# Kernel tuning notes

Hardware: AMD Instinct MI355X
Metric: run time of the kernel (lower is better)

## Reference

```python
import jax, jax.numpy as jnp
import numpy as np

L = 8        # n_layers (coupling layers)
H = 128      # hidden width
B = 262144   # batch
BN_EPS = 1e-5
FLOW_EPS = 1e-4


def setup_inputs() -> dict:
    key = jax.random.key(0)
    ks = jax.random.split(key, 16)
    d = {}
    d['x'] = jax.random.normal(ks[0], (B, 2), dtype=jnp.float32)
    # weight-normalized Linear(1 -> H): direction v, magnitude g, bias b
    d['v1'] = jax.random.normal(ks[1], (L, H, 1), dtype=jnp.float32)
    d['g1'] = 1.0 + 0.1 * jax.random.normal(ks[2], (L, H), dtype=jnp.float32)
    d['b1'] = 0.1 * jax.random.normal(ks[3], (L, H), dtype=jnp.float32)
    d['bn1_g'] = 1.0 + 0.1 * jax.random.normal(ks[4], (L, H), dtype=jnp.float32)
    d['bn1_b'] = 0.1 * jax.random.normal(ks[5], (L, H), dtype=jnp.float32)
    # weight-normalized Linear(H -> H)
    d['v2'] = jax.random.normal(ks[6], (L, H, H), dtype=jnp.float32) / np.sqrt(H)
    d['g2'] = 1.0 + 0.1 * jax.random.normal(ks[7], (L, H), dtype=jnp.float32)
    d['b2'] = 0.1 * jax.random.normal(ks[8], (L, H), dtype=jnp.float32)
    d['bn2_g'] = 1.0 + 0.1 * jax.random.normal(ks[9], (L, H), dtype=jnp.float32)
    d['bn2_b'] = 0.1 * jax.random.normal(ks[10], (L, H), dtype=jnp.float32)
    # final plain Linear(H -> 2)
    d['wf'] = jax.random.normal(ks[11], (L, 2, H), dtype=jnp.float32) / np.sqrt(H)
    d['bf'] = 0.1 * jax.random.normal(ks[12], (L, 2), dtype=jnp.float32)
    return d


def _wn_linear(x, v, g, b):
    # torch weight_norm: W = g * v / ||v||_row  (norm over input dim)
    w = g[:, None] * v / jnp.linalg.norm(v, axis=1, keepdims=True)  # [out, in]
    return x @ w.T + b


def _bn_train(h, gamma, beta):
    # BatchNorm1d training-mode math: batch mean / biased batch var
    m = h.mean(axis=0)
    va = h.var(axis=0)
    return (h - m) * jax.lax.rsqrt(va + BN_EPS) * gamma + beta


def reference(x, v1, g1, b1, bn1_g, bn1_b, v2, g2, b2, bn2_g, bn2_b, wf, bf):
    rev = (jnp.arange(L) % 2 == 0)  # mask_reversed for layer i

    def step(carry, layer):
        xc, sldj = carry
        (lv1, lg1, lb1, lbg1, lbb1, lv2, lg2, lb2, lbg2, lbb2, lwf, lbf, lrev) = layer
        x0 = xc[:, :1]
        x1 = xc[:, 1:]
        xin = jnp.where(lrev, x1, x0)   # conditioning half
        xo = jnp.where(lrev, x0, x1)    # transformed half
        h = jax.nn.relu(_bn_train(_wn_linear(xin, lv1, lg1, lb1), lbg1, lbb1))
        h = jax.nn.relu(_bn_train(_wn_linear(h, lv2, lg2, lb2), lbg2, lbb2))
        st = h @ lwf.T + lbf            # [B, 2]
        s = jnp.tanh(st[:, :1])
        t = st[:, 1:]
        y = jnp.exp(s) * xo + t
        out = jnp.where(lrev,
                        jnp.concatenate([y, x1], axis=-1),
                        jnp.concatenate([x0, y], axis=-1))
        return (out, sldj + s[:, 0]), None

    init = (x, jnp.zeros((x.shape[0],), dtype=x.dtype))
    xs = (v1, g1, b1, bn1_g, bn1_b, v2, g2, b2, bn2_g, bn2_b, wf, bf, rev)
    (y, sldj), _ = jax.lax.scan(step, init, xs)
    z = jax.nn.sigmoid(y)
    sldj = sldj + jnp.log(z * (1.0 - z) + FLOW_EPS).sum(axis=-1)
    return z, sldj
```

## Files before the change

kernel.cpp:

```cpp
#include <hip/hip_runtime.h>
#include <math.h>


#define BN_ 262144
#define H_ 128
#define NBINS 129

#define OFF_STAT 0
#define OFF_PM   128
#define OFF_TS   16512
#define OFF_XP   16640
#define OFF_SL   (OFF_XP + 2*BN_)
#define OFF_KB   (OFF_XP + 3*BN_)
#define OFF_V2T  (OFF_KB + BN_/4)
#define OFF_WSC  (OFF_V2T + 8*H_*H_)
#define OFF_S    (OFF_WSC + 8*H_)
#define OFF_UP   (OFF_S + NBINS*H_*2)
#define OFF_U    (OFF_UP + NBINS*8)
#define OFF_C    (OFF_U + NBINS*H_)

__device__ __forceinline__ float4 bsum4(float4 v, volatile float* tmp, int tid) {
    for (int off = 32; off; off >>= 1) {
        v.x += __shfl_down(v.x, off); v.y += __shfl_down(v.y, off);
        v.z += __shfl_down(v.z, off); v.w += __shfl_down(v.w, off);
    }
    if ((tid & 63) == 0) {
        int w = (tid >> 6) * 4;
        tmp[w] = v.x; tmp[w+1] = v.y; tmp[w+2] = v.z; tmp[w+3] = v.w;
    }
    __syncthreads();
    float4 r = make_float4(tmp[0]+tmp[4], tmp[1]+tmp[5],
                           tmp[2]+tmp[6], tmp[3]+tmp[7]);
    __syncthreads();
    return r;
}

__global__ __launch_bounds__(1024) void k_init(const float* __restrict__ x,
    const float* __restrict__ v2, const float* __restrict__ g2,
    float* __restrict__ ws) {
    const int tid = threadIdx.x;
    __shared__ float rs[16], rss[16], w2[16];
    int b = blockIdx.x * 1024 + tid;
    float2 xv = ((const float2*)x)[b];
    float s1 = xv.y, s2 = xv.y * xv.y;
    for (int off = 32; off; off >>= 1) {
        s1 += __shfl_down(s1, off); s2 += __shfl_down(s2, off);
    }
    if ((tid & 63) == 0) { rs[tid>>6] = s1; rss[tid>>6] = s2; }
    __syncthreads();
    if (tid == 0) {
        float a = 0.f, c = 0.f;
        for (int w = 0; w < 16; w++) { a += rs[w]; c += rss[w]; }
        atomicAdd(&ws[OFF_STAT + (blockIdx.x & 7)*2], a);
        atomicAdd(&ws[OFF_STAT + (blockIdx.x & 7)*2 + 1], c);
    }
    if (blockIdx.x < 128) {
        const int l = blockIdx.x >> 4, i0 = (blockIdx.x & 15) * 8;
        const int iloc = tid >> 7, j = tid & 127;
        float val = v2[(l*H_ + i0 + iloc)*H_ + j];
        ws[OFF_V2T + (l*H_ + j)*H_ + i0 + iloc] = val;
        float s = val * val;
        for (int off = 32; off; off >>= 1) s += __shfl_down(s, off);
        if ((tid & 63) == 0) w2[tid >> 6] = s;
        __syncthreads();
        if (tid < 8)
            ws[OFF_WSC + l*H_ + i0 + tid] =
                g2[l*H_ + i0 + tid] / sqrtf(w2[2*tid] + w2[2*tid+1]);
    }
}

__global__ __launch_bounds__(1024, 4) void k_bin(
    const float* __restrict__ x,
    const float* __restrict__ v1, const float* __restrict__ g1,
    const float* __restrict__ bn1g, const float* __restrict__ bn1b,
    const float* __restrict__ b2,
    float* __restrict__ ws, int l, int rev) {
    __shared__ float sA[H_], sC[H_], sTun[H_], sTs[H_], wscs[H_], b2s[H_];
    __shared__ int ordr[H_];
    __shared__ float pT1[8][H_], pT0[8][H_], pB1[8][H_], pB0[8][H_];
    __shared__ float scratch[5216];
    float* lb = scratch + 2048;
    const int tid = threadIdx.x;
    const int i = tid & 127, cc = tid >> 7;
    const float* v2T = ws + OFF_V2T + l*H_*H_;
    const int b = blockIdx.x * 1024 + tid;

    float xin;
    if (l == 0) xin = ((const float2*)x)[b].y;
    else {
        float2 xp = ((const float2*)(ws + OFF_XP))[b];
        xin = rev ? xp.y : xp.x;
    }

    if (tid < H_) {
        float Ssum = 0.f, SSq = 0.f;
        #pragma unroll
        for (int s = 0; s < 8; ++s) {
            Ssum += ws[OFF_STAT + l*16 + 2*s];
            SSq  += ws[OFF_STAT + l*16 + 2*s + 1];
        }
        float mx = Ssum * (1.f / BN_);
        float vx = fmaxf(SSq * (1.f / BN_) - mx * mx, 0.f);
        float g1v = g1[l*H_ + tid];
        float w1 = (v1[l*H_ + tid] >= 0.f) ? g1v : -g1v;
        float r = rsqrtf(vx * g1v * g1v + 1e-5f);
        float a = w1 * r * bn1g[l*H_ + tid];
        float c = bn1b[l*H_ + tid] - mx * a;
        sA[tid] = a; sC[tid] = c;
        sTun[tid] = (a != 0.f) ? (-c / a) : 3.0e38f;
        wscs[tid] = ws[OFF_WSC + l*H_ + tid];
        b2s[tid] = b2[l*H_ + tid];
    }
    for (int e = tid; e < 3168; e += 1024) lb[e] = 0.f;
    __syncthreads();
    {
        int* prank = (int*)scratch;
        float tj = sTun[i];
        int pr = 0;
        #pragma unroll
        for (int m = 0; m < 16; ++m) {
            int q = cc*16 + m;
            float tq = sTun[q];
            pr += (tq < tj || (tq == tj && q < i)) ? 1 : 0;
        }
        prank[cc*128 + i] = pr;
        __syncthreads();
        if (tid < H_) {
            int rk = 0;
            #pragma unroll
            for (int s = 0; s < 8; ++s) rk += prank[s*128 + tid];
            ordr[rk] = tid;
            float tv = sTun[tid];
            sTs[rk] = tv;
            if (blockIdx.x == 0) ws[OFF_TS + rk] = tv;
        }
    }
    __syncthreads();
    float rT1_[16];
    {
        int pos = 0;
        #pragma unroll
        for (int s = 64; s; s >>= 1) pos += (sTs[pos + s - 1] < xin) ? s : 0;
        pos += (sTs[pos] < xin) ? 1 : 0;
        ((unsigned char*)(ws + OFF_KB))[b] = (unsigned char)pos;
        float* lbr = lb + (tid & 7) * 396;
        atomicAdd(&lbr[pos], 1.f);
        atomicAdd(&lbr[132 + pos], xin);
        atomicAdd(&lbr[264 + pos], xin * xin);

        float b1 = 0.f, b0 = 0.f, t1 = 0.f, t0 = 0.f;
        #pragma unroll
        for (int m = 0; m < 16; ++m) {
            int jm = ordr[cc*16 + m];
            float am = sA[jm], cm = sC[jm];
            float vm = v2T[jm*H_ + i];
            if ((am < 0.f) || (am == 0.f && cm > 0.f)) { b1 += vm*am; b0 += vm*cm; }
            float d1 = 0.f;
            if (am != 0.f) {
                float sg = (am > 0.f) ? 1.f : -1.f;
                d1 = sg*vm*am; t0 += sg*vm*cm;
            }
            rT1_[m] = d1; t1 += d1;
        }
        pT1[cc][i] = t1; pT0[cc][i] = t0; pB1[cc][i] = b1; pB0[cc][i] = b0;
    }
    __syncthreads();
    if (tid < 396) {
        float v = lb[tid];
        #pragma unroll
        for (int c = 1; c < 8; ++c) v += lb[c*396 + tid];
        lb[tid] = v;
    }
    __syncthreads();
    {
        float S1 = 0.f, S0 = 0.f;
        #pragma unroll
        for (int c2 = 0; c2 < 8; ++c2) {
            S1 += pB1[c2][i]; S0 += pB0[c2][i];
            if (c2 < cc) { S1 += pT1[c2][i]; S0 += pT0[c2][i]; }
        }
        float wsci = wscs[i], b2i = b2s[i];
        float pm = 0.f, pe = 0.f;
        float2* STg = (float2*)(ws + OFF_S);
        #pragma unroll
        for (int r = 0; r < 16; ++r) {
            int k = 16*cc + r;
            float cn = lb[k], sx = lb[132 + k], sxx = lb[264 + k];
            float A = wsci * S1;
            float B = fmaf(wsci, S0, b2i);
            if (blockIdx.x == 0) STg[k*H_ + i] = make_float2(A, B);
            pm += A*sx + B*cn;
            pe += A*A*sxx + 2.f*A*B*sx + B*B*cn;
            float d1 = rT1_[r];
            S1 += d1;
            S0 = fmaf(-d1, sTs[16*cc + r], S0);
        }
        if (cc == 7) {
            float cn = lb[128], sx = lb[260], sxx = lb[392];
            float A = wsci * S1;
            float B = fmaf(wsci, S0, b2i);
            if (blockIdx.x == 0) STg[128*H_ + i] = make_float2(A, B);
            pm += A*sx + B*cn;
            pe += A*A*sxx + 2.f*A*B*sx + B*B*cn;
        }
        float* red1 = scratch;
        float* red2 = scratch + 1024;
        red1[tid] = pm; red2[tid] = pe;
        __syncthreads();
        if (tid < H_) {
            float m = 0.f, e2 = 0.f;
            #pragma unroll
            for (int c2 = 0; c2 < 8; ++c2) {
                m += red1[c2*128 + tid]; e2 += red2[c2*128 + tid];
            }
            int slot = blockIdx.x & 7;
            atomicAdd(&ws[OFF_PM + l*2048 + slot*256 + tid], m);
            atomicAdd(&ws[OFF_PM + l*2048 + slot*256 + 128 + tid], e2);
        }
    }
}

__global__ __launch_bounds__(128) void k_prep2(
    const float* __restrict__ bn2g, const float* __restrict__ bn2b,
    const float* __restrict__ wf, const float* __restrict__ bf,
    float* __restrict__ ws, int l) {
    const int j = threadIdx.x, k = blockIdx.x;
    __shared__ float skey[H_], sval[H_];
    __shared__ float4 sc4[H_];
    __shared__ float red[8];
    float2 mys = ((const float2*)(ws + OFF_S))[k*H_ + j];
    float lo = (k > 0) ? ws[OFF_TS + k - 1] : -INFINITY;
    float hi = (k < NBINS - 1) ? ws[OFF_TS + k] : INFINITY;
    float w0 = wf[l*2*H_ + j], w1 = wf[l*2*H_ + H_ + j];
    float bg = bn2g[l*H_ + j], bb2 = bn2b[l*H_ + j];
    float pmv = 0.f, pev = 0.f;
    #pragma unroll
    for (int s = 0; s < 8; ++s) {
        pmv += ws[OFF_PM + l*2048 + s*256 + j];
        pev += ws[OFF_PM + l*2048 + s*256 + 128 + j];
    }
    float mean = pmv * (1.f / BN_);
    float var = fmaxf(pev * (1.f / BN_) - mean * mean, 0.f);
    float R = bg * rsqrtf(var + 1e-5f);
    float a = mys.x * R;
    float c = (mys.y - mean) * R + bb2;
    bool actv = (k == 0) ? ((a < 0.f) || (a == 0.f && c > 0.f))
                         : (fmaf(a, lo, c) > 0.f);
    float u = (a != 0.f) ? (-c / a) : INFINITY;
    bool rel = (a != 0.f) && (u > lo) && (u < hi);
    float key = rel ? u : INFINITY;
    skey[j] = key;
    __syncthreads();
    int rk = 0;
    for (int q = 0; q < H_; q++) {
        float kq = skey[q];
        rk += ((kq < key) || (kq == key && q < j)) ? 1 : 0;
    }
    float4 bb = bsum4(actv ? make_float4(w0*a, w0*c, w1*a, w1*c)
                           : make_float4(0.f, 0.f, 0.f, 0.f), red, j);
    float sg = rel ? ((a > 0.f) ? 1.f : -1.f) : 0.f;
    sval[rk] = key;
    sc4[rk] = make_float4(sg*w0*a, sg*w0*c, sg*w1*a, sg*w1*c);
    __syncthreads();
    for (int off = 1; off < H_; off <<= 1) {
        float4 add = (j >= off) ? sc4[j - off] : make_float4(0.f, 0.f, 0.f, 0.f);
        __syncthreads();
        sc4[j].x += add.x; sc4[j].y += add.y; sc4[j].z += add.z; sc4[j].w += add.w;
        __syncthreads();
    }
    float bfx = bf[2*l], bfy = bf[2*l + 1];
    ws[OFF_U + k*H_ + j] = sval[j];
    if (j < 8) ws[OFF_UP + k*8 + j] = sval[16*j + 15];
    float4* Cg = (float4*)(ws + OFF_C) + k * 132;
    float4 sj = sc4[j];
    Cg[j + 1] = make_float4(bb.x + sj.x, bb.y + bfx + sj.y,
                            bb.z + sj.z, bb.w + bfy + sj.w);
    if (j == 0) Cg[0] = make_float4(bb.x, bb.y + bfx, bb.z, bb.w + bfy);
}

__global__ __launch_bounds__(1024) void k_step(
    const float* __restrict__ x,
    float* __restrict__ ws, float* __restrict__ out,
    int l, int rev, int last) {
    __shared__ float4 lup4[NBINS * 2];
    __shared__ float rsc[32];
    const int tid = threadIdx.x;
    const int b = blockIdx.x * 1024 + tid;
    int kb = ((const unsigned char*)(ws + OFF_KB))[b];
    float x0v, x1v, sl;
    if (l == 0) {
        float2 xv = ((const float2*)x)[b];
        x0v = xv.x; x1v = xv.y; sl = 0.f;
    } else {
        float2 xp = ((const float2*)(ws + OFF_XP))[b];
        x0v = xp.x; x1v = xp.y; sl = ws[OFF_SL + b];
    }
    float* lup = (float*)lup4;
    for (int e = tid; e < NBINS * 8; e += 1024) lup[e] = ws[OFF_UP + e];
    __syncthreads();
    float xin = rev ? x1v : x0v;
    float xo  = rev ? x0v : x1v;
    float4 p0 = lup4[kb*2], p1 = lup4[kb*2 + 1];
    int s16 = (p0.x<xin)+(p0.y<xin)+(p0.z<xin)+(p0.w<xin)
            + (p1.x<xin)+(p1.y<xin)+(p1.z<xin)+(p1.w<xin);
    if (s16 > 7) s16 = 7;
    const float4* Ur = (const float4*)(ws + OFF_U + kb*H_ + s16*16);
    float4 q0 = Ur[0], q1 = Ur[1], q2 = Ur[2], q3 = Ur[3];
    int c2 = (q0.x<xin)+(q0.y<xin)+(q0.z<xin)+(q0.w<xin)
           + (q1.x<xin)+(q1.y<xin)+(q1.z<xin)+(q1.w<xin)
           + (q2.x<xin)+(q2.y<xin)+(q2.z<xin)+(q2.w<xin)
           + (q3.x<xin)+(q3.y<xin)+(q3.z<xin)+(q3.w<xin);
    int s = s16 * 16 + c2;
    float4 C = ((const float4*)(ws + OFF_C))[kb*132 + s];
    float stx = fmaf(C.x, xin, C.y);
    float sty = fmaf(C.z, xin, C.w);
    float sv = tanhf(stx);
    float y = expf(sv) * xo + sty;
    sl += sv;
    if (!last) {
        float nx0 = rev ? y : x0v;
        float nx1 = rev ? x1v : y;
        ((float2*)(ws + OFF_XP))[b] = make_float2(nx0, nx1);
        ws[OFF_SL + b] = sl;
        float s1 = y, s2 = y * y;
        for (int off = 32; off; off >>= 1) {
            s1 += __shfl_down(s1, off); s2 += __shfl_down(s2, off);
        }
        int lane = tid & 63, wid = tid >> 6;
        if (lane == 0) { rsc[wid] = s1; rsc[16 + wid] = s2; }
        __syncthreads();
        if (tid == 0) {
            float aa = 0.f, cc = 0.f;
            for (int w = 0; w < 16; w++) { aa += rsc[w]; cc += rsc[16 + w]; }
            int slot = blockIdx.x & 7;
            atomicAdd(&ws[OFF_STAT + (l+1)*16 + slot*2], aa);
            atomicAdd(&ws[OFF_STAT + (l+1)*16 + slot*2 + 1], cc);
        }
    } else {
        float z0 = 1.f / (1.f + expf(-x0v));
        float z1 = 1.f / (1.f + expf(-y));
        ((float2*)out)[b] = make_float2(z0, z1);
        out[2*BN_ + b] = sl + logf(z0 * (1.f - z0) + 1e-4f)
                            + logf(z1 * (1.f - z1) + 1e-4f);
    }
}

extern "C" void kernel_launch(void* const* d_in, const int* in_sizes, int n_in,
                              void* d_out, int out_size, void* d_ws, size_t ws_size,
                              hipStream_t stream) {
    const float* x    = (const float*)d_in[0];
    const float* v1   = (const float*)d_in[1];
    const float* g1   = (const float*)d_in[2];
    const float* bn1g = (const float*)d_in[4];
    const float* bn1b = (const float*)d_in[5];
    const float* v2   = (const float*)d_in[6];
    const float* g2   = (const float*)d_in[7];
    const float* b2   = (const float*)d_in[8];
    const float* bn2g = (const float*)d_in[9];
    const float* bn2b = (const float*)d_in[10];
    const float* wf   = (const float*)d_in[11];
    const float* bf   = (const float*)d_in[12];
    float* ws  = (float*)d_ws;
    float* out = (float*)d_out;

    hipMemsetAsync(ws, 0, 16512 * sizeof(float), stream);
    k_init<<<256, 1024, 0, stream>>>(x, v2, g2, ws);
    for (int l = 0; l < 8; l++) {
        int rev = (l % 2 == 0) ? 1 : 0;
        int last = (l == 7) ? 1 : 0;
        k_bin<<<256, 1024, 0, stream>>>(x, v1, g1, bn1g, bn1b, b2, ws, l, rev);
        k_prep2<<<NBINS, 128, 0, stream>>>(bn2g, bn2b, wf, bf, ws, l);
        k_step<<<256, 1024, 0, stream>>>(x, ws, out, l, rev, last);
    }
}
```

Measured before the change: 348.1 us.

## Bucket samples by first-layer bin and evaluate second layer directly per bin

The per-bin breakpoint sorting kernel (k_prep2) and the per-sample two-level breakpoint search are removed. k_bin now counting-sorts sample indices by first-layer bin, and k_step walks samples in bin order, building per-bin second-layer coefficients in shared memory and evaluating all 128 ReLU units with an explicit loop. This drops one launch per layer and the scan-heavy prep work, but adds 128 FMAs per sample, indirect gathers and scatters through an index array, and extra scans over per-block counts.

Result: slower. 486.5 us (+39.7%).

```diff
diff --git a/kernel.cpp b/kernel.cpp
--- a/kernel.cpp
+++ b/kernel.cpp
@@ -7,33 +7,16 @@
 #define NBINS 129
 
 #define OFF_STAT 0
-#define OFF_PM   128
-#define OFF_TS   16512
-#define OFF_XP   16640
-#define OFF_SL   (OFF_XP + 2*BN_)
-#define OFF_KB   (OFF_XP + 3*BN_)
-#define OFF_V2T  (OFF_KB + BN_/4)
-#define OFF_WSC  (OFF_V2T + 8*H_*H_)
-#define OFF_S    (OFF_WSC + 8*H_)
-#define OFF_UP   (OFF_S + NBINS*H_*2)
-#define OFF_U    (OFF_UP + NBINS*8)
-#define OFF_C    (OFF_U + NBINS*H_)
-
-__device__ __forceinline__ float4 bsum4(float4 v, volatile float* tmp, int tid) {
-    for (int off = 32; off; off >>= 1) {
-        v.x += __shfl_down(v.x, off); v.y += __shfl_down(v.y, off);
-        v.z += __shfl_down(v.z, off); v.w += __shfl_down(v.w, off);
-    }
-    if ((tid & 63) == 0) {
-        int w = (tid >> 6) * 4;
-        tmp[w] = v.x; tmp[w+1] = v.y; tmp[w+2] = v.z; tmp[w+3] = v.w;
-    }
-    __syncthreads();
-    float4 r = make_float4(tmp[0]+tmp[4], tmp[1]+tmp[5],
-                           tmp[2]+tmp[6], tmp[3]+tmp[7]);
-    __syncthreads();
-    return r;
-}
+#define OFF_PM   256
+#define OFF_GBC  16640
+#define OFF_CNT  17696
+#define OFF_OFS  51488
+#define OFF_IDX  85280
+#define OFF_XP   347424
+#define OFF_SL   871712
+#define OFF_V2T  1133856
+#define OFF_WSC  1264928
+#define OFF_S    1265952
 
 __global__ __launch_bounds__(1024) void k_init(const float* __restrict__ x,
     const float* __restrict__ v2, const float* __restrict__ g2,
@@ -51,8 +34,8 @@
     if (tid == 0) {
         float a = 0.f, c = 0.f;
         for (int w = 0; w < 16; w++) { a += rs[w]; c += rss[w]; }
-        atomicAdd(&ws[OFF_STAT + (blockIdx.x & 7)*2], a);
-        atomicAdd(&ws[OFF_STAT + (blockIdx.x & 7)*2 + 1], c);
+        atomicAdd(&ws[OFF_STAT + (blockIdx.x & 15)*2], a);
+        atomicAdd(&ws[OFF_STAT + (blockIdx.x & 15)*2 + 1], c);
     }
     if (blockIdx.x < 128) {
         const int l = blockIdx.x >> 4, i0 = (blockIdx.x & 15) * 8;
@@ -79,6 +62,7 @@
     __shared__ int ordr[H_];
     __shared__ float pT1[8][H_], pT0[8][H_], pB1[8][H_], pB0[8][H_];
     __shared__ float scratch[5216];
+    __shared__ int binTotI[132], sBase[132];
     float* lb = scratch + 2048;
     const int tid = threadIdx.x;
     const int i = tid & 127, cc = tid >> 7;
@@ -95,9 +79,9 @@
     if (tid < H_) {
         float Ssum = 0.f, SSq = 0.f;
         #pragma unroll
-        for (int s = 0; s < 8; ++s) {
-            Ssum += ws[OFF_STAT + l*16 + 2*s];
-            SSq  += ws[OFF_STAT + l*16 + 2*s + 1];
+        for (int s = 0; s < 16; ++s) {
+            Ssum += ws[OFF_STAT + l*32 + 2*s];
+            SSq  += ws[OFF_STAT + l*32 + 2*s + 1];
         }
         float mx = Ssum * (1.f / BN_);
         float vx = fmaxf(SSq * (1.f / BN_) - mx * mx, 0.f);
@@ -130,21 +114,20 @@
             #pragma unroll
             for (int s = 0; s < 8; ++s) rk += prank[s*128 + tid];
             ordr[rk] = tid;
-            float tv = sTun[tid];
-            sTs[rk] = tv;
-            if (blockIdx.x == 0) ws[OFF_TS + rk] = tv;
+            sTs[rk] = sTun[tid];
         }
     }
     __syncthreads();
     float rT1_[16];
+    int pos, rnk;
     {
-        int pos = 0;
-        #pragma unroll
-        for (int s = 64; s; s >>= 1) pos += (sTs[pos + s - 1] < xin) ? s : 0;
-        pos += (sTs[pos] < xin) ? 1 : 0;
-        ((unsigned char*)(ws + OFF_KB))[b] = (unsigned char)pos;
+        int p = 0;
+        #pragma unroll
+        for (int s = 64; s; s >>= 1) p += (sTs[p + s - 1] < xin) ? s : 0;
+        p += (sTs[p] < xin) ? 1 : 0;
+        pos = p;
         float* lbr = lb + (tid & 7) * 396;
-        atomicAdd(&lbr[pos], 1.f);
+        rnk = (int)atomicAdd(&lbr[pos], 1.f);
         atomicAdd(&lbr[132 + pos], xin);
         atomicAdd(&lbr[264 + pos], xin * xin);
 
@@ -165,13 +148,52 @@
         pT1[cc][i] = t1; pT0[cc][i] = t0; pB1[cc][i] = b1; pB0[cc][i] = b0;
     }
     __syncthreads();
-    if (tid < 396) {
+    if (tid < NBINS) {
+        int p = 0;
+        #pragma unroll
+        for (int c = 0; c < 8; ++c) {
+            int cv = (int)lb[c*396 + tid];
+            lb[c*396 + tid] = (float)p;
+            p += cv;
+        }
+        binTotI[tid] = p;
+    } else if (tid >= 132 && tid < 396) {
         float v = lb[tid];
         #pragma unroll
         for (int c = 1; c < 8; ++c) v += lb[c*396 + tid];
         lb[tid] = v;
     }
     __syncthreads();
+    if (tid < 64) {
+        int v0 = binTotI[tid], v1 = binTotI[64 + tid];
+        int s0 = v0;
+        #pragma unroll
+        for (int off = 1; off < 64; off <<= 1) {
+            int u = __shfl_up(s0, off); if (tid >= off) s0 += u;
+        }
+        int t0 = __shfl(s0, 63);
+        int s1v = v1;
+        #pragma unroll
+        for (int off = 1; off < 64; off <<= 1) {
+            int u = __shfl_up(s1v, off); if (tid >= off) s1v += u;
+        }
+        s1v += t0;
+        int t1 = __shfl(s1v, 63);
+        sBase[tid] = s0 - v0;
+        sBase[64 + tid] = s1v - v1;
+        if (tid == 0) sBase[128] = t1;
+    }
+    __syncthreads();
+    {
+        int slotPref = (int)lb[(tid & 7)*396 + pos];
+        int myOfs = sBase[pos] + slotPref + rnk;
+        ((int*)ws)[OFF_IDX + blockIdx.x*1024 + myOfs] = b;
+        if (tid < NBINS) {
+            ((int*)ws)[OFF_CNT + tid*256 + blockIdx.x] = binTotI[tid];
+            ((int*)ws)[OFF_OFS + tid*256 + blockIdx.x] = sBase[tid];
+            atomicAdd(((int*)ws) + OFF_GBC + l*132 + tid, binTotI[tid]);
+        }
+    }
     {
         float S1 = 0.f, S0 = 0.f;
         #pragma unroll
@@ -185,7 +207,7 @@
         #pragma unroll
         for (int r = 0; r < 16; ++r) {
             int k = 16*cc + r;
-            float cn = lb[k], sx = lb[132 + k], sxx = lb[264 + k];
+            float cn = (float)binTotI[k], sx = lb[132 + k], sxx = lb[264 + k];
             float A = wsci * S1;
             float B = fmaf(wsci, S0, b2i);
             if (blockIdx.x == 0) STg[k*H_ + i] = make_float2(A, B);
@@ -196,7 +218,7 @@
             S0 = fmaf(-d1, sTs[16*cc + r], S0);
         }
         if (cc == 7) {
-            float cn = lb[128], sx = lb[260], sxx = lb[392];
+            float cn = (float)binTotI[128], sx = lb[260], sxx = lb[392];
             float A = wsci * S1;
             float B = fmaf(wsci, S0, b2i);
             if (blockIdx.x == 0) STg[128*H_ + i] = make_float2(A, B);
@@ -220,128 +242,141 @@
     }
 }
 
-__global__ __launch_bounds__(128) void k_prep2(
+__global__ __launch_bounds__(256) void k_step(
+    const float* __restrict__ x,
     const float* __restrict__ bn2g, const float* __restrict__ bn2b,
     const float* __restrict__ wf, const float* __restrict__ bf,
-    float* __restrict__ ws, int l) {
-    const int j = threadIdx.x, k = blockIdx.x;
-    __shared__ float skey[H_], sval[H_];
-    __shared__ float4 sc4[H_];
-    __shared__ float red[8];
-    float2 mys = ((const float2*)(ws + OFF_S))[k*H_ + j];
-    float lo = (k > 0) ? ws[OFF_TS + k - 1] : -INFINITY;
-    float hi = (k < NBINS - 1) ? ws[OFF_TS + k] : INFINITY;
-    float w0 = wf[l*2*H_ + j], w1 = wf[l*2*H_ + H_ + j];
-    float bg = bn2g[l*H_ + j], bb2 = bn2b[l*H_ + j];
-    float pmv = 0.f, pev = 0.f;
-    #pragma unroll
-    for (int s = 0; s < 8; ++s) {
-        pmv += ws[OFF_PM + l*2048 + s*256 + j];
-        pev += ws[OFF_PM + l*2048 + s*256 + 128 + j];
-    }
-    float mean = pmv * (1.f / BN_);
-    float var = fmaxf(pev * (1.f / BN_) - mean * mean, 0.f);
-    float R = bg * rsqrtf(var + 1e-5f);
-    float a = mys.x * R;
-    float c = (mys.y - mean) * R + bb2;
-    bool actv = (k == 0) ? ((a < 0.f) || (a == 0.f && c > 0.f))
-                         : (fmaf(a, lo, c) > 0.f);
-    float u = (a != 0.f) ? (-c / a) : INFINITY;
-    bool rel = (a != 0.f) && (u > lo) && (u < hi);
-    float key = rel ? u : INFINITY;
-    skey[j] = key;
-    __syncthreads();
-    int rk = 0;
-    for (int q = 0; q < H_; q++) {
-        float kq = skey[q];
-        rk += ((kq < key) || (kq == key && q < j)) ? 1 : 0;
-    }
-    float4 bb = bsum4(actv ? make_float4(w0*a, w0*c, w1*a, w1*c)
-                           : make_float4(0.f, 0.f, 0.f, 0.f), red, j);
-    float sg = rel ? ((a > 0.f) ? 1.f : -1.f) : 0.f;
-    sval[rk] = key;
-    sc4[rk] = make_float4(sg*w0*a, sg*w0*c, sg*w1*a, sg*w1*c);
-    __syncthreads();
-    for (int off = 1; off < H_; off <<= 1) {
-        float4 add = (j >= off) ? sc4[j - off] : make_float4(0.f, 0.f, 0.f, 0.f);
-        __syncthreads();
-        sc4[j].x += add.x; sc4[j].y += add.y; sc4[j].z += add.z; sc4[j].w += add.w;
-        __syncthreads();
-    }
-    float bfx = bf[2*l], bfy = bf[2*l + 1];
-    ws[OFF_U + k*H_ + j] = sval[j];
-    if (j < 8) ws[OFF_UP + k*8 + j] = sval[16*j + 15];
-    float4* Cg = (float4*)(ws + OFF_C) + k * 132;
-    float4 sj = sc4[j];
-    Cg[j + 1] = make_float4(bb.x + sj.x, bb.y + bfx + sj.y,
-                            bb.z + sj.z, bb.w + bfy + sj.w);
-    if (j == 0) Cg[0] = make_float4(bb.x, bb.y + bfx, bb.z, bb.w + bfy);
-}
-
-__global__ __launch_bounds__(1024) void k_step(
-    const float* __restrict__ x,
     float* __restrict__ ws, float* __restrict__ out,
     int l, int rev, int last) {
-    __shared__ float4 lup4[NBINS * 2];
-    __shared__ float rsc[32];
-    const int tid = threadIdx.x;
-    const int b = blockIdx.x * 1024 + tid;
-    int kb = ((const unsigned char*)(ws + OFF_KB))[b];
-    float x0v, x1v, sl;
-    if (l == 0) {
-        float2 xv = ((const float2*)x)[b];
-        x0v = xv.x; x1v = xv.y; sl = 0.f;
-    } else {
-        float2 xp = ((const float2*)(ws + OFF_XP))[b];
-        x0v = xp.x; x1v = xp.y; sl = ws[OFF_SL + b];
-    }
-    float* lup = (float*)lup4;
-    for (int e = tid; e < NBINS * 8; e += 1024) lup[e] = ws[OFF_UP + e];
-    __syncthreads();
-    float xin = rev ? x1v : x0v;
-    float xo  = rev ? x0v : x1v;
-    float4 p0 = lup4[kb*2], p1 = lup4[kb*2 + 1];
-    int s16 = (p0.x<xin)+(p0.y<xin)+(p0.z<xin)+(p0.w<xin)
-            + (p1.x<xin)+(p1.y<xin)+(p1.z<xin)+(p1.w<xin);
-    if (s16 > 7) s16 = 7;
-    const float4* Ur = (const float4*)(ws + OFF_U + kb*H_ + s16*16);
-    float4 q0 = Ur[0], q1 = Ur[1], q2 = Ur[2], q3 = Ur[3];
-    int c2 = (q0.x<xin)+(q0.y<xin)+(q0.z<xin)+(q0.w<xin)
-           + (q1.x<xin)+(q1.y<xin)+(q1.z<xin)+(q1.w<xin)
-           + (q2.x<xin)+(q2.y<xin)+(q2.z<xin)+(q2.w<xin)
-           + (q3.x<xin)+(q3.y<xin)+(q3.z<xin)+(q3.w<xin);
-    int s = s16 * 16 + c2;
-    float4 C = ((const float4*)(ws + OFF_C))[kb*132 + s];
-    float stx = fmaf(C.x, xin, C.y);
-    float sty = fmaf(C.z, xin, C.w);
-    float sv = tanhf(stx);
-    float y = expf(sv) * xo + sty;
-    sl += sv;
+    __shared__ int sG[256];
+    __shared__ int sCp[256];
+    __shared__ int sOfs[256];
+    __shared__ int wtot[4];
+    __shared__ float4 af4[H_];
+    __shared__ float2 rmb[H_];
+    __shared__ int kk[2];
+    __shared__ float rsc[8];
+    const int tid = threadIdx.x, lane = tid & 63, wid = tid >> 6;
+
+    int g = (tid < NBINS) ? ((const int*)ws)[OFF_GBC + l*132 + tid] : 0;
+    int sg = g;
+    #pragma unroll
+    for (int off = 1; off < 64; off <<= 1) {
+        int u = __shfl_up(sg, off); if (lane >= off) sg += u;
+    }
+    if (lane == 63) wtot[wid] = sg;
+    __syncthreads();
+    int carry = 0;
+    for (int w = 0; w < wid; ++w) carry += wtot[w];
+    sg += carry;
+    sG[tid] = sg;
+    __syncthreads();
+    const int r = blockIdx.x * 256 + tid;
+    int myk = 0;
+    #pragma unroll
+    for (int st = 128; st; st >>= 1)
+        if (myk + st <= NBINS && sG[myk + st - 1] <= r) myk += st;
+    if (tid == 0) kk[0] = myk;
+    if (tid == 255) kk[1] = myk;
+    float wf0 = 0.f, wf1 = 0.f;
+    if (tid < H_) {
+        float pmv = 0.f, pev = 0.f;
+        #pragma unroll
+        for (int s = 0; s < 8; ++s) {
+            pmv += ws[OFF_PM + l*2048 + s*256 + tid];
+            pev += ws[OFF_PM + l*2048 + s*256 + 128 + tid];
+        }
+        float mean = pmv * (1.f / BN_);
+        float var = fmaxf(pev * (1.f / BN_) - mean * mean, 0.f);
+        float R = bn2g[l*H_ + tid] * rsqrtf(var + 1e-5f);
+        rmb[tid] = make_float2(R, fmaf(-mean, R, bn2b[l*H_ + tid]));
+        wf0 = wf[l*2*H_ + tid]; wf1 = wf[l*2*H_ + H_ + tid];
+    }
+    __syncthreads();
+    const int k0 = kk[0], k1 = kk[1];
+    const float2* STg = (const float2*)(ws + OFF_S);
+    float bfx = bf[2*l], bfy = bf[2*l + 1];
+    float y = 0.f;
+    for (int k = k0; k <= k1; ++k) {
+        int gk = sG[k] - (k ? sG[k-1] : 0);
+        if (gk == 0) continue;
+        __syncthreads();
+        int cv = ((const int*)ws)[OFF_CNT + k*256 + tid];
+        int ov = ((const int*)ws)[OFF_OFS + k*256 + tid];
+        int sc = cv;
+        #pragma unroll
+        for (int off = 1; off < 64; off <<= 1) {
+            int u = __shfl_up(sc, off); if (lane >= off) sc += u;
+        }
+        if (lane == 63) wtot[wid] = sc;
+        __syncthreads();
+        int cr = 0;
+        for (int w = 0; w < wid; ++w) cr += wtot[w];
+        sc += cr;
+        sCp[tid] = sc; sOfs[tid] = ov;
+        if (tid < H_) {
+            float2 st2 = STg[k*H_ + tid];
+            float2 rb = rmb[tid];
+            af4[tid] = make_float4(st2.x * rb.x, fmaf(st2.y, rb.x, rb.y), wf0, wf1);
+        }
+        __syncthreads();
+        if (myk == k) {
+            int rr = r - (k ? sG[k-1] : 0);
+            int bl = 0;
+            #pragma unroll
+            for (int st = 128; st; st >>= 1)
+                if (bl + st <= 256 && sCp[bl + st - 1] <= rr) bl += st;
+            int within = rr - (bl ? sCp[bl-1] : 0);
+            int smp = ((const int*)ws)[OFF_IDX + (bl << 10) + sOfs[bl] + within];
+            float x0v, x1v, sl;
+            if (l == 0) {
+                float2 xv = ((const float2*)x)[smp];
+                x0v = xv.x; x1v = xv.y; sl = 0.f;
+            } else {
+                float2 xp = ((const float2*)(ws + OFF_XP))[smp];
+                x0v = xp.x; x1v = xp.y; sl = ws[OFF_SL + smp];
+            }
+            float xin = rev ? x1v : x0v;
+            float xo  = rev ? x0v : x1v;
+            float stx = bfx, sty = bfy;
+            #pragma unroll 8
+            for (int i2 = 0; i2 < H_; ++i2) {
+                float4 q = af4[i2];
+                float h = fmaxf(fmaf(xin, q.x, q.y), 0.f);
+                stx = fmaf(q.z, h, stx);
+                sty = fmaf(q.w, h, sty);
+            }
+            float sv = tanhf(stx);
+            y = expf(sv) * xo + sty;
+            sl += sv;
+            if (!last) {
+                float nx0 = rev ? y : x0v;
+                float nx1 = rev ? x1v : y;
+                ((float2*)(ws + OFF_XP))[smp] = make_float2(nx0, nx1);
+                ws[OFF_SL + smp] = sl;
+            } else {
+                float z0 = 1.f / (1.f + expf(-x0v));
+                float z1 = 1.f / (1.f + expf(-y));
+                ((float2*)out)[smp] = make_float2(z0, z1);
+                out[2*BN_ + smp] = sl + logf(z0 * (1.f - z0) + 1e-4f)
+                                      + logf(z1 * (1.f - z1) + 1e-4f);
+            }
+        }
+    }
     if (!last) {
-        float nx0 = rev ? y : x0v;
-        float nx1 = rev ? x1v : y;
-        ((float2*)(ws + OFF_XP))[b] = make_float2(nx0, nx1);
-        ws[OFF_SL + b] = sl;
         float s1 = y, s2 = y * y;
         for (int off = 32; off; off >>= 1) {
             s1 += __shfl_down(s1, off); s2 += __shfl_down(s2, off);
         }
-        int lane = tid & 63, wid = tid >> 6;
-        if (lane == 0) { rsc[wid] = s1; rsc[16 + wid] = s2; }
+        if (lane == 0) { rsc[wid] = s1; rsc[4 + wid] = s2; }
         __syncthreads();
         if (tid == 0) {
-            float aa = 0.f, cc = 0.f;
-            for (int w = 0; w < 16; w++) { aa += rsc[w]; cc += rsc[16 + w]; }
-            int slot = blockIdx.x & 7;
-            atomicAdd(&ws[OFF_STAT + (l+1)*16 + slot*2], aa);
-            atomicAdd(&ws[OFF_STAT + (l+1)*16 + slot*2 + 1], cc);
-        }
-    } else {
-        float z0 = 1.f / (1.f + expf(-x0v));
-        float z1 = 1.f / (1.f + expf(-y));
-        ((float2*)out)[b] = make_float2(z0, z1);
-        out[2*BN_ + b] = sl + logf(z0 * (1.f - z0) + 1e-4f)
-                            + logf(z1 * (1.f - z1) + 1e-4f);
+            float aa = 0.f, cc2 = 0.f;
+            for (int w = 0; w < 4; ++w) { aa += rsc[w]; cc2 += rsc[4 + w]; }
+            int slot = blockIdx.x & 15;
+            atomicAdd(&ws[OFF_STAT + (l+1)*32 + slot*2], aa);
+            atomicAdd(&ws[OFF_STAT + (l+1)*32 + slot*2 + 1], cc2);
+        }
     }
 }
 
@@ -363,13 +398,13 @@
     float* ws  = (float*)d_ws;
     float* out = (float*)d_out;
 
-    hipMemsetAsync(ws, 0, 16512 * sizeof(float), stream);
+    hipMemsetAsync(ws, 0, 17696 * sizeof(float), stream);
     k_init<<<256, 1024, 0, stream>>>(x, v2, g2, ws);
     for (int l = 0; l < 8; l++) {
         int rev = (l % 2 == 0) ? 1 : 0;
         int last = (l == 7) ? 1 : 0;
         k_bin<<<256, 1024, 0, stream>>>(x, v1, g1, bn1g, bn1b, b2, ws, l, rev);
-        k_prep2<<<NBINS, 128, 0, stream>>>(bn2g, bn2b, wf, bf, ws, l);
-        k_step<<<256, 1024, 0, stream>>>(x, ws, out, l, rev, last);
+        k_step<<<1024, 256, 0, stream>>>(x, bn2g, bn2b, wf, bf, ws, out,
+                                         l, rev, last);
     }
 }
```

## Fuse per-bin prep2 into k_bin tail via last-blocks atomic counter

Applied to the files above, without the earlier changes.

Removes the separate k_prep2 launch per layer. The last 8 blocks of k_bin to finish spin on a global arrival counter until all 256 blocks have published their BN2 partial sums. They then build the per-bin sorted breakpoints and prefix-sum tables, 8 bins at a time with 1024 threads. This saves one launch and one dependency gap per layer, at the cost of relying on all blocks being co-resident for the spin-wait and using more shared memory per block.

After: 495.7 us. 42.4% more time.

```diff
diff --git a/kernel.cpp b/kernel.cpp
--- a/kernel.cpp
+++ b/kernel.cpp
@@ -8,7 +8,7 @@
 
 #define OFF_STAT 0
 #define OFF_PM   128
-#define OFF_TS   16512
+#define OFF_CNT  16512
 #define OFF_XP   16640
 #define OFF_SL   (OFF_XP + 2*BN_)
 #define OFF_KB   (OFF_XP + 3*BN_)
@@ -19,20 +19,19 @@
 #define OFF_U    (OFF_UP + NBINS*8)
 #define OFF_C    (OFF_U + NBINS*H_)
 
-__device__ __forceinline__ float4 bsum4(float4 v, volatile float* tmp, int tid) {
-    for (int off = 32; off; off >>= 1) {
-        v.x += __shfl_down(v.x, off); v.y += __shfl_down(v.y, off);
-        v.z += __shfl_down(v.z, off); v.w += __shfl_down(v.w, off);
-    }
-    if ((tid & 63) == 0) {
-        int w = (tid >> 6) * 4;
-        tmp[w] = v.x; tmp[w+1] = v.y; tmp[w+2] = v.z; tmp[w+3] = v.w;
-    }
-    __syncthreads();
-    float4 r = make_float4(tmp[0]+tmp[4], tmp[1]+tmp[5],
-                           tmp[2]+tmp[6], tmp[3]+tmp[7]);
-    __syncthreads();
-    return r;
+__device__ __forceinline__ void cst2(float* p, float2 v) {
+    __hip_atomic_store((unsigned long long*)p,
+                       __builtin_bit_cast(unsigned long long, v),
+                       __ATOMIC_RELAXED, __HIP_MEMORY_SCOPE_AGENT);
+}
+__device__ __forceinline__ float2 ald2(const float* p) {
+    unsigned long long u = __hip_atomic_load((unsigned long long*)p,
+                       __ATOMIC_RELAXED, __HIP_MEMORY_SCOPE_AGENT);
+    return __builtin_bit_cast(float2, u);
+}
+__device__ __forceinline__ float ald(const float* p) {
+    return __hip_atomic_load((float*)p, __ATOMIC_RELAXED,
+                             __HIP_MEMORY_SCOPE_AGENT);
 }
 
 __global__ __launch_bounds__(1024) void k_init(const float* __restrict__ x,
@@ -74,11 +73,17 @@
     const float* __restrict__ v1, const float* __restrict__ g1,
     const float* __restrict__ bn1g, const float* __restrict__ bn1b,
     const float* __restrict__ b2,
+    const float* __restrict__ bn2g, const float* __restrict__ bn2b,
+    const float* __restrict__ wf, const float* __restrict__ bf,
     float* __restrict__ ws, int l, int rev) {
     __shared__ float sA[H_], sC[H_], sTun[H_], sTs[H_], wscs[H_], b2s[H_];
     __shared__ int ordr[H_];
-    __shared__ float pT1[8][H_], pT0[8][H_], pB1[8][H_], pB0[8][H_];
+    __shared__ float pbuf[4096];
+    __shared__ float scanB[4096];
     __shared__ float scratch[5216];
+    __shared__ int stayS;
+    float* pT1p = pbuf;       float* pT0p = pbuf + 1024;
+    float* pB1p = pbuf + 2048; float* pB0p = pbuf + 3072;
     float* lb = scratch + 2048;
     const int tid = threadIdx.x;
     const int i = tid & 127, cc = tid >> 7;
@@ -130,9 +135,7 @@
             #pragma unroll
             for (int s = 0; s < 8; ++s) rk += prank[s*128 + tid];
             ordr[rk] = tid;
-            float tv = sTun[tid];
-            sTs[rk] = tv;
-            if (blockIdx.x == 0) ws[OFF_TS + rk] = tv;
+            sTs[rk] = sTun[tid];
         }
     }
     __syncthreads();
@@ -162,7 +165,8 @@
             }
             rT1_[m] = d1; t1 += d1;
         }
-        pT1[cc][i] = t1; pT0[cc][i] = t0; pB1[cc][i] = b1; pB0[cc][i] = b0;
+        pT1p[cc*128+i] = t1; pT0p[cc*128+i] = t0;
+        pB1p[cc*128+i] = b1; pB0p[cc*128+i] = b0;
     }
     __syncthreads();
     if (tid < 396) {
@@ -176,19 +180,19 @@
         float S1 = 0.f, S0 = 0.f;
         #pragma unroll
         for (int c2 = 0; c2 < 8; ++c2) {
-            S1 += pB1[c2][i]; S0 += pB0[c2][i];
-            if (c2 < cc) { S1 += pT1[c2][i]; S0 += pT0[c2][i]; }
+            S1 += pB1p[c2*128+i]; S0 += pB0p[c2*128+i];
+            if (c2 < cc) { S1 += pT1p[c2*128+i]; S0 += pT0p[c2*128+i]; }
         }
         float wsci = wscs[i], b2i = b2s[i];
         float pm = 0.f, pe = 0.f;
-        float2* STg = (float2*)(ws + OFF_S);
+        float* STg = ws + OFF_S;
         #pragma unroll
         for (int r = 0; r < 16; ++r) {
             int k = 16*cc + r;
             float cn = lb[k], sx = lb[132 + k], sxx = lb[264 + k];
             float A = wsci * S1;
             float B = fmaf(wsci, S0, b2i);
-            if (blockIdx.x == 0) STg[k*H_ + i] = make_float2(A, B);
+            if (blockIdx.x == 0) cst2(STg + 2*(k*H_ + i), make_float2(A, B));
             pm += A*sx + B*cn;
             pe += A*A*sxx + 2.f*A*B*sx + B*B*cn;
             float d1 = rT1_[r];
@@ -199,7 +203,7 @@
             float cn = lb[128], sx = lb[260], sxx = lb[392];
             float A = wsci * S1;
             float B = fmaf(wsci, S0, b2i);
-            if (blockIdx.x == 0) STg[128*H_ + i] = make_float2(A, B);
+            if (blockIdx.x == 0) cst2(STg + 2*(128*H_ + i), make_float2(A, B));
             pm += A*sx + B*cn;
             pe += A*A*sxx + 2.f*A*B*sx + B*B*cn;
         }
@@ -218,64 +222,113 @@
             atomicAdd(&ws[OFF_PM + l*2048 + slot*256 + 128 + tid], e2);
         }
     }
-}
-
-__global__ __launch_bounds__(128) void k_prep2(
-    const float* __restrict__ bn2g, const float* __restrict__ bn2b,
-    const float* __restrict__ wf, const float* __restrict__ bf,
-    float* __restrict__ ws, int l) {
-    const int j = threadIdx.x, k = blockIdx.x;
-    __shared__ float skey[H_], sval[H_];
-    __shared__ float4 sc4[H_];
-    __shared__ float red[8];
-    float2 mys = ((const float2*)(ws + OFF_S))[k*H_ + j];
-    float lo = (k > 0) ? ws[OFF_TS + k - 1] : -INFINITY;
-    float hi = (k < NBINS - 1) ? ws[OFF_TS + k] : INFINITY;
-    float w0 = wf[l*2*H_ + j], w1 = wf[l*2*H_ + H_ + j];
-    float bg = bn2g[l*H_ + j], bb2 = bn2b[l*H_ + j];
-    float pmv = 0.f, pev = 0.f;
-    #pragma unroll
-    for (int s = 0; s < 8; ++s) {
-        pmv += ws[OFF_PM + l*2048 + s*256 + j];
-        pev += ws[OFF_PM + l*2048 + s*256 + 128 + j];
-    }
-    float mean = pmv * (1.f / BN_);
-    float var = fmaxf(pev * (1.f / BN_) - mean * mean, 0.f);
-    float R = bg * rsqrtf(var + 1e-5f);
-    float a = mys.x * R;
-    float c = (mys.y - mean) * R + bb2;
-    bool actv = (k == 0) ? ((a < 0.f) || (a == 0.f && c > 0.f))
-                         : (fmaf(a, lo, c) > 0.f);
-    float u = (a != 0.f) ? (-c / a) : INFINITY;
-    bool rel = (a != 0.f) && (u > lo) && (u < hi);
-    float key = rel ? u : INFINITY;
-    skey[j] = key;
-    __syncthreads();
-    int rk = 0;
-    for (int q = 0; q < H_; q++) {
-        float kq = skey[q];
-        rk += ((kq < key) || (kq == key && q < j)) ? 1 : 0;
-    }
-    float4 bb = bsum4(actv ? make_float4(w0*a, w0*c, w1*a, w1*c)
-                           : make_float4(0.f, 0.f, 0.f, 0.f), red, j);
-    float sg = rel ? ((a > 0.f) ? 1.f : -1.f) : 0.f;
-    sval[rk] = key;
-    sc4[rk] = make_float4(sg*w0*a, sg*w0*c, sg*w1*a, sg*w1*c);
-    __syncthreads();
-    for (int off = 1; off < H_; off <<= 1) {
-        float4 add = (j >= off) ? sc4[j - off] : make_float4(0.f, 0.f, 0.f, 0.f);
-        __syncthreads();
-        sc4[j].x += add.x; sc4[j].y += add.y; sc4[j].z += add.z; sc4[j].w += add.w;
-        __syncthreads();
-    }
-    float bfx = bf[2*l], bfy = bf[2*l + 1];
-    ws[OFF_U + k*H_ + j] = sval[j];
-    if (j < 8) ws[OFF_UP + k*8 + j] = sval[16*j + 15];
-    float4* Cg = (float4*)(ws + OFF_C) + k * 132;
-    float4 sj = sc4[j];
-    Cg[j + 1] = make_float4(bb.x + sj.x, bb.y + bfx + sj.y,
-                            bb.z + sj.z, bb.w + bfy + sj.w);
-    if (j == 0) Cg[0] = make_float4(bb.x, bb.y + bfx, bb.z, bb.w + bfy);
+    __syncthreads();
+    if (tid == 0) {
+        int old = atomicAdd((int*)ws + OFF_CNT + l, 1);
+        stayS = old - 248;
+    }
+    __syncthreads();
+    const int si = stayS;
+    if (si < 0) return;
+    if (tid == 0) {
+        while (__hip_atomic_load((int*)ws + OFF_CNT + l, __ATOMIC_RELAXED,
+                                 __HIP_MEMORY_SCOPE_AGENT) < 256)
+            __builtin_amdgcn_s_sleep(2);
+    }
+    __syncthreads();
+    float* sR  = scratch;       float* sMean = scratch + 128;
+    float* sW0 = scratch + 256; float* sW1 = scratch + 384;
+    float* sB2 = scratch + 512;
+    float* skey8 = scratch + 640;
+    float* sval8 = scratch + 1664;
+    float* gred  = scratch + 2688;
+    if (tid < H_) {
+        float pmv = 0.f, pev = 0.f;
+        #pragma unroll
+        for (int s = 0; s < 8; ++s) {
+            pmv += ald(ws + OFF_PM + l*2048 + s*256 + tid);
+            pev += ald(ws + OFF_PM + l*2048 + s*256 + 128 + tid);
+        }
+        float mean = pmv * (1.f / BN_);
+        float var = fmaxf(pev * (1.f / BN_) - mean * mean, 0.f);
+        sR[tid] = bn2g[l*H_ + tid] * rsqrtf(var + 1e-5f);
+        sMean[tid] = mean;
+        sB2[tid] = bn2b[l*H_ + tid];
+        sW0[tid] = wf[l*2*H_ + tid];
+        sW1[tid] = wf[l*2*H_ + H_ + tid];
+    }
+    __syncthreads();
+    const float bfx = bf[2*l], bfy = bf[2*l + 1];
+    const int g = tid >> 7, j = tid & 127;
+    const int kbase = si * 17;
+    const int kend = (kbase + 17 < NBINS) ? kbase + 17 : NBINS;
+    const float w0 = sW0[j], w1 = sW1[j];
+    for (int k0i = kbase; k0i < kend; k0i += 8) {
+        const int k = k0i + g;
+        const bool act = (k < kend);
+        float a = 0.f, c = 0.f, key = INFINITY;
+        bool rel = false, actv = false;
+        if (act) {
+            float2 mys = ald2(ws + OFF_S + 2*(k*H_ + j));
+            float R = sR[j];
+            a = mys.x * R;
+            c = (mys.y - sMean[j]) * R + sB2[j];
+            float lo = (k > 0) ? sTs[k - 1] : -INFINITY;
+            float hi = (k < NBINS - 1) ? sTs[k] : INFINITY;
+            actv = (k == 0) ? ((a < 0.f) || (a == 0.f && c > 0.f))
+                            : (fmaf(a, lo, c) > 0.f);
+            float u = (a != 0.f) ? (-c / a) : INFINITY;
+            rel = (a != 0.f) && (u > lo) && (u < hi);
+            key = rel ? u : INFINITY;
+        }
+        skey8[g*128 + j] = key;
+        __syncthreads();
+        int rk = 0;
+        for (int q = 0; q < H_; q++) {
+            float kq = skey8[g*128 + q];
+            rk += ((kq < key) || (kq == key && q < j)) ? 1 : 0;
+        }
+        float4 v = (act && actv) ? make_float4(w0*a, w0*c, w1*a, w1*c)
+                                 : make_float4(0.f, 0.f, 0.f, 0.f);
+        for (int off = 32; off; off >>= 1) {
+            v.x += __shfl_down(v.x, off); v.y += __shfl_down(v.y, off);
+            v.z += __shfl_down(v.z, off); v.w += __shfl_down(v.w, off);
+        }
+        if ((tid & 63) == 0) {
+            int w = (tid >> 6) * 4;
+            gred[w] = v.x; gred[w+1] = v.y; gred[w+2] = v.z; gred[w+3] = v.w;
+        }
+        __syncthreads();
+        float4 bb = make_float4(gred[(2*g)*4]   + gred[(2*g+1)*4],
+                                gred[(2*g)*4+1] + gred[(2*g+1)*4+1],
+                                gred[(2*g)*4+2] + gred[(2*g+1)*4+2],
+                                gred[(2*g)*4+3] + gred[(2*g+1)*4+3]);
+        float sg = rel ? ((a > 0.f) ? 1.f : -1.f) : 0.f;
+        float4* cur = (float4*)pbuf;
+        float4* nxt = (float4*)scanB;
+        sval8[g*128 + rk] = key;
+        cur[g*128 + rk] = make_float4(sg*w0*a, sg*w0*c, sg*w1*a, sg*w1*c);
+        __syncthreads();
+        for (int off = 1; off < H_; off <<= 1) {
+            float4 add = (j >= off) ? cur[g*128 + j - off]
+                                    : make_float4(0.f, 0.f, 0.f, 0.f);
+            float4 cv = cur[g*128 + j];
+            nxt[g*128 + j] = make_float4(cv.x + add.x, cv.y + add.y,
+                                         cv.z + add.z, cv.w + add.w);
+            __syncthreads();
+            float4* t = cur; cur = nxt; nxt = t;
+        }
+        if (act) {
+            float4 sj = cur[g*128 + j];
+            ws[OFF_U + k*H_ + j] = sval8[g*128 + j];
+            if (j < 8) ws[OFF_UP + k*8 + j] = sval8[g*128 + 16*j + 15];
+            float4* Cg = (float4*)(ws + OFF_C) + k * 132;
+            Cg[j + 1] = make_float4(bb.x + sj.x, bb.y + bfx + sj.y,
+                                    bb.z + sj.z, bb.w + bfy + sj.w);
+            if (j == 0) Cg[0] = make_float4(bb.x, bb.y + bfx, bb.z, bb.w + bfy);
+        }
+        __syncthreads();
+    }
 }
 
 __global__ __launch_bounds__(1024) void k_step(
@@ -363,13 +416,13 @@
     float* ws  = (float*)d_ws;
     float* out = (float*)d_out;
 
-    hipMemsetAsync(ws, 0, 16512 * sizeof(float), stream);
+    hipMemsetAsync(ws, 0, 16640 * sizeof(float), stream);
     k_init<<<256, 1024, 0, stream>>>(x, v2, g2, ws);
     for (int l = 0; l < 8; l++) {
         int rev = (l % 2 == 0) ? 1 : 0;
         int last = (l == 7) ? 1 : 0;
-        k_bin<<<256, 1024, 0, stream>>>(x, v1, g1, bn1g, bn1b, b2, ws, l, rev);
-        k_prep2<<<NBINS, 128, 0, stream>>>(bn2g, bn2b, wf, bf, ws, l);
+        k_bin<<<256, 1024, 0, stream>>>(x, v1, g1, bn1g, bn1b, b2,
+                                        bn2g, bn2b, wf, bf, ws, l, rev);
         k_step<<<256, 1024, 0, stream>>>(x, ws, out, l, rev, last);
     }
 }
```

## Pack per-sample x and log-det into float4 and precompute sorted activation coefficients

Applied to the files above, without the earlier changes.

Merges the separate x-pair and sldj workspace arrays into a single interleaved float4 per sample, so each step does one vector load and one vector store instead of a float2 plus a scalar. In k_bin, the sign- and activity-dependent coefficients are precomputed once per hidden unit in rank order, which removes the branches and indirect a/c lookups from the inner accumulation loop. The trade-off is that the float4 carries an unused padding lane, which raises k_step's read and write traffic from 12 to 16 bytes per sample.

New measurement: 326.8 us. 1.07x faster.

```diff
diff --git a/kernel.cpp b/kernel.cpp
--- a/kernel.cpp
+++ b/kernel.cpp
@@ -9,15 +9,14 @@
 #define OFF_STAT 0
 #define OFF_PM   128
 #define OFF_TS   16512
-#define OFF_XP   16640
-#define OFF_SL   (OFF_XP + 2*BN_)
-#define OFF_KB   (OFF_XP + 3*BN_)
-#define OFF_V2T  (OFF_KB + BN_/4)
-#define OFF_WSC  (OFF_V2T + 8*H_*H_)
-#define OFF_S    (OFF_WSC + 8*H_)
-#define OFF_UP   (OFF_S + NBINS*H_*2)
-#define OFF_U    (OFF_UP + NBINS*8)
-#define OFF_C    (OFF_U + NBINS*H_)
+#define OFF_XQ   16640
+#define OFF_KB   1065216
+#define OFF_V2T  1130752
+#define OFF_WSC  1261824
+#define OFF_S    1262848
+#define OFF_UP   1295872
+#define OFF_U    1296904
+#define OFF_C    1313416
 
 __device__ __forceinline__ float4 bsum4(float4 v, volatile float* tmp, int tid) {
     for (int off = 32; off; off >>= 1) {
@@ -75,7 +74,8 @@
     const float* __restrict__ bn1g, const float* __restrict__ bn1b,
     const float* __restrict__ b2,
     float* __restrict__ ws, int l, int rev) {
-    __shared__ float sA[H_], sC[H_], sTun[H_], sTs[H_], wscs[H_], b2s[H_];
+    __shared__ float sTun[H_], sTs[H_], wscs[H_], b2s[H_];
+    __shared__ float ta[H_], tc[H_], ba[H_], bc[H_];
     __shared__ int ordr[H_];
     __shared__ float pT1[8][H_], pT0[8][H_], pB1[8][H_], pB0[8][H_];
     __shared__ float scratch[5216];
@@ -88,10 +88,11 @@
     float xin;
     if (l == 0) xin = ((const float2*)x)[b].y;
     else {
-        float2 xp = ((const float2*)(ws + OFF_XP))[b];
-        xin = rev ? xp.y : xp.x;
-    }
-
+        float4 xq = ((const float4*)(ws + OFF_XQ))[b];
+        xin = rev ? xq.y : xq.x;
+    }
+
+    float a = 0.f, c = 0.f, tj = 0.f;
     if (tid < H_) {
         float Ssum = 0.f, SSq = 0.f;
         #pragma unroll
@@ -104,10 +105,10 @@
         float g1v = g1[l*H_ + tid];
         float w1 = (v1[l*H_ + tid] >= 0.f) ? g1v : -g1v;
         float r = rsqrtf(vx * g1v * g1v + 1e-5f);
-        float a = w1 * r * bn1g[l*H_ + tid];
-        float c = bn1b[l*H_ + tid] - mx * a;
-        sA[tid] = a; sC[tid] = c;
-        sTun[tid] = (a != 0.f) ? (-c / a) : 3.0e38f;
+        a = w1 * r * bn1g[l*H_ + tid];
+        c = bn1b[l*H_ + tid] - mx * a;
+        tj = (a != 0.f) ? (-c / a) : 3.0e38f;
+        sTun[tid] = tj;
         wscs[tid] = ws[OFF_WSC + l*H_ + tid];
         b2s[tid] = b2[l*H_ + tid];
     }
@@ -115,13 +116,13 @@
     __syncthreads();
     {
         int* prank = (int*)scratch;
-        float tj = sTun[i];
+        float tq0 = sTun[i];
         int pr = 0;
         #pragma unroll
         for (int m = 0; m < 16; ++m) {
             int q = cc*16 + m;
             float tq = sTun[q];
-            pr += (tq < tj || (tq == tj && q < i)) ? 1 : 0;
+            pr += (tq < tq0 || (tq == tq0 && q < i)) ? 1 : 0;
         }
         prank[cc*128 + i] = pr;
         __syncthreads();
@@ -130,9 +131,15 @@
             #pragma unroll
             for (int s = 0; s < 8; ++s) rk += prank[s*128 + tid];
             ordr[rk] = tid;
-            float tv = sTun[tid];
-            sTs[rk] = tv;
-            if (blockIdx.x == 0) ws[OFF_TS + rk] = tv;
+            sTs[rk] = tj;
+            if (blockIdx.x == 0) ws[OFF_TS + rk] = tj;
+            float sg = (a > 0.f) ? 1.f : -1.f;
+            bool nz = (a != 0.f);
+            ta[rk] = nz ? sg * a : 0.f;
+            tc[rk] = nz ? sg * c : 0.f;
+            bool act = (a < 0.f) || (a == 0.f && c > 0.f);
+            ba[rk] = act ? a : 0.f;
+            bc[rk] = act ? c : 0.f;
         }
     }
     __syncthreads();
@@ -151,15 +158,12 @@
         float b1 = 0.f, b0 = 0.f, t1 = 0.f, t0 = 0.f;
         #pragma unroll
         for (int m = 0; m < 16; ++m) {
-            int jm = ordr[cc*16 + m];
-            float am = sA[jm], cm = sC[jm];
-            float vm = v2T[jm*H_ + i];
-            if ((am < 0.f) || (am == 0.f && cm > 0.f)) { b1 += vm*am; b0 += vm*cm; }
-            float d1 = 0.f;
-            if (am != 0.f) {
-                float sg = (am > 0.f) ? 1.f : -1.f;
-                d1 = sg*vm*am; t0 += sg*vm*cm;
-            }
+            int sm = cc*16 + m;
+            float vm = v2T[ordr[sm]*H_ + i];
+            b1 = fmaf(vm, ba[sm], b1);
+            b0 = fmaf(vm, bc[sm], b0);
+            float d1 = vm * ta[sm];
+            t0 = fmaf(vm, tc[sm], t0);
             rT1_[m] = d1; t1 += d1;
         }
         pT1[cc][i] = t1; pT0[cc][i] = t0; pB1[cc][i] = b1; pB0[cc][i] = b0;
@@ -168,7 +172,7 @@
     if (tid < 396) {
         float v = lb[tid];
         #pragma unroll
-        for (int c = 1; c < 8; ++c) v += lb[c*396 + tid];
+        for (int c2 = 1; c2 < 8; ++c2) v += lb[c2*396 + tid];
         lb[tid] = v;
     }
     __syncthreads();
@@ -292,8 +296,8 @@
         float2 xv = ((const float2*)x)[b];
         x0v = xv.x; x1v = xv.y; sl = 0.f;
     } else {
-        float2 xp = ((const float2*)(ws + OFF_XP))[b];
-        x0v = xp.x; x1v = xp.y; sl = ws[OFF_SL + b];
+        float4 xq = ((const float4*)(ws + OFF_XQ))[b];
+        x0v = xq.x; x1v = xq.y; sl = xq.z;
     }
     float* lup = (float*)lup4;
     for (int e = tid; e < NBINS * 8; e += 1024) lup[e] = ws[OFF_UP + e];
@@ -320,8 +324,7 @@
     if (!last) {
         float nx0 = rev ? y : x0v;
         float nx1 = rev ? x1v : y;
-        ((float2*)(ws + OFF_XP))[b] = make_float2(nx0, nx1);
-        ws[OFF_SL + b] = sl;
+        ((float4*)(ws + OFF_XQ))[b] = make_float4(nx0, nx1, sl, 0.f);
         float s1 = y, s2 = y * y;
         for (int off = 32; off; off >>= 1) {
             s1 += __shfl_down(s1, off); s2 += __shfl_down(s2, off);
```
